# Kernel optimization log

Hardware: AMD Instinct MI355X
Metric: run time of the kernel (lower is better)

Reference implementation:

```python
import jax, jax.numpy as jnp
import numpy as np

B, C, H, W = 16, 192, 64, 64
L = 256           # number of quantization levels (len(sos.unique_values))
EXTREMA = 10.0    # codebook support roughly [-extrema, extrema]


def setup_inputs() -> dict:
    key = jax.random.key(0)
    k1, k2, k3 = jax.random.split(key, 3)
    inputs = jax.random.normal(k1, (B, C, H, W), dtype=jnp.float32) * 3.0
    means = jax.random.normal(k2, (B, C, H, W), dtype=jnp.float32)
    # sorted codebook of unique quantizer output values (sos.unique_values)
    raw = jax.random.uniform(k3, (L,), dtype=jnp.float32,
                             minval=-EXTREMA, maxval=EXTREMA)
    unique_values = jnp.sort(raw)
    return {"inputs": inputs, "means": means, "unique_values": unique_values}


def _nearest_symbols(v, unique_values):
    # Parallel binary search over the sorted codebook; equivalent to the
    # original per-element argmin(|keys - x|) in transform_map.
    L_ = unique_values.shape[0]
    idx = jnp.searchsorted(unique_values, v)          # in [0, L]
    idx = jnp.clip(idx, 1, L_ - 1)
    left = unique_values[idx - 1]
    right = unique_values[idx]
    # on ties, argmin picks the lower index -> use <=
    return jnp.where(jnp.abs(v - left) <= jnp.abs(v - right), idx - 1, idx)


def reference(inputs, means, unique_values):
    # quantize(mode='symbols'): subtract means, snap to nearest codebook
    # value, map value -> integer symbol via the sorted codebook.
    v = inputs - means
    symbols = _nearest_symbols(v, unique_values)      # int32 [B,C,H,W]
    # dequantize: symbol -> float codebook value (map_cdf_sos), add means.
    dequant = unique_values[symbols] + means          # float32 [B,C,H,W]
    return dequant, symbols
```

## Files before the change

### kernel.cpp

```cpp
#include <hip/hip_runtime.h>


#define LVL 256
#define NB  512
#define QPT 4

typedef float f32x4 __attribute__((ext_vector_type(4)));

__device__ __forceinline__ int bucket_of(float v, float lo, float scale) {
    int b = (int)floorf((v - lo) * scale);
    return min(max(b, 0), NB - 1);
}

__global__ __launch_bounds__(256) void agc_build_lut(
    const float* __restrict__ uv, float4* __restrict__ lutA, float4* __restrict__ lutB)
{
    __shared__ float s_uv[LVL];
    __shared__ int   s_b[LVL];
    int t = threadIdx.x;
    s_uv[t] = uv[t];
    __syncthreads();
    const float lo    = s_uv[0];
    const float scale = (float)NB / (s_uv[LVL - 1] - lo);
    s_b[t] = bucket_of(s_uv[t], lo, scale);
    __syncthreads();

    int b = blockIdx.x * 256 + t;
    if (b >= NB) return;

    int A = 0, cnt = 0;
    for (int j = 0; j < LVL; ++j) {
        int bj = s_b[j];
        A   += (bj <  b);
        cnt += (bj == b);
    }

    const float INF = __builtin_inff();
    float4 ea, eb;
    if (cnt == 0) {
        int idx = min(max(A, 1), LVL - 1);
        ea = make_float4(INF, INF, s_uv[idx - 1], s_uv[idx]);
        eb = make_float4(0.f, 0.f, 0.f, __int_as_float(idx - 1));
    } else if (cnt <= 2 && A >= 1 && A + cnt <= LVL - 1) {
        float p0 = s_uv[A];
        float p1 = (cnt >= 2) ? s_uv[A + 1] : INF;
        float c0 = s_uv[A - 1];
        float c1 = s_uv[A];
        float c2 = s_uv[A + 1];
        float c3 = (A + 2 <= LVL - 1) ? s_uv[A + 2] : 0.f;
        ea = make_float4(p0, p1, c0, c1);
        eb = make_float4(c2, c3, 0.f, __int_as_float(A - 1));
    } else {
        ea = make_float4(0.f, 0.f, 0.f, 0.f);
        eb = make_float4(0.f, 0.f, 0.f, __int_as_float(-(A + 1)));
    }
    lutA[b] = ea;
    lutB[b] = eb;
}

__global__ __launch_bounds__(256) void agc_quant_lut(
    const float* __restrict__ inputs,
    const float* __restrict__ means,
    const float* __restrict__ uv,
    const f32x4* __restrict__ lutA,
    const f32x4* __restrict__ lutB,
    float* __restrict__ out_deq,
    float* __restrict__ out_sym,
    int n4, int n, int nfull)
{
    const float lo    = uv[0];
    const float scale = (float)NB / (uv[LVL - 1] - lo);

    int t = threadIdx.x;
    const int i0 = blockIdx.x * (256 * QPT) + t;
    const bool full = (blockIdx.x < nfull);

    f32x4 in[QPT], mn[QPT];
    if (full) {
        #pragma unroll
        for (int k = 0; k < QPT; ++k) {
            int i = i0 + k * 256;
            in[k] = __builtin_nontemporal_load(reinterpret_cast<const f32x4*>(inputs) + i);
            mn[k] = __builtin_nontemporal_load(reinterpret_cast<const f32x4*>(means) + i);
        }
    } else {
        #pragma unroll
        for (int k = 0; k < QPT; ++k) {
            int i = i0 + k * 256;
            if (i < n4) {
                in[k] = __builtin_nontemporal_load(reinterpret_cast<const f32x4*>(inputs) + i);
                mn[k] = __builtin_nontemporal_load(reinterpret_cast<const f32x4*>(means) + i);
            }
        }
    }

    #pragma unroll
    for (int k = 0; k < QPT; ++k) {
        int i = i0 + k * 256;
        if (!full && i >= n4) continue;

        float vs[4] = {in[k].x - mn[k].x, in[k].y - mn[k].y,
                       in[k].z - mn[k].z, in[k].w - mn[k].w};
        float ms[4] = {mn[k].x, mn[k].y, mn[k].z, mn[k].w};
        float dq[4], sy[4];

        int bx[4];
        #pragma unroll
        for (int e = 0; e < 4; ++e) bx[e] = bucket_of(vs[e], lo, scale);

        f32x4 A4[4], B4[4];
        #pragma unroll
        for (int e = 0; e < 4; ++e) {
            A4[e] = lutA[bx[e]];
            B4[e] = lutB[bx[e]];
        }

        #pragma unroll
        for (int e = 0; e < 4; ++e) {
            float v = vs[e];
            int bp = __float_as_int(B4[e].w);

            float left, right;
            int base;
            if (bp >= 0) {
                int sel = (A4[e].x < v) + (A4[e].y < v);
                left  = (sel == 0) ? A4[e].z : ((sel == 1) ? A4[e].w : B4[e].x);
                right = (sel == 0) ? A4[e].w : ((sel == 1) ? B4[e].x : B4[e].y);
                base  = bp + sel;
            } else {
                int s = -bp - 1;
                while (s < LVL && uv[s] < v) ++s;
                int idx = min(max(s, 1), LVL - 1);
                left  = uv[idx - 1];
                right = uv[idx];
                base  = idx - 1;
            }

            bool tl = (fabsf(v - left) <= fabsf(v - right));
            sy[e] = (float)(base + (tl ? 0 : 1));
            dq[e] = (tl ? left : right) + ms[e];
        }

        reinterpret_cast<float4*>(out_deq)[i] = make_float4(dq[0], dq[1], dq[2], dq[3]);
        reinterpret_cast<float4*>(out_sym)[i] = make_float4(sy[0], sy[1], sy[2], sy[3]);
    }

    if (blockIdx.x == 0 && t == 0) {
        for (int j = n4 * 4; j < n; ++j) {
            float m = means[j];
            float v = inputs[j] - m;
            int l = 0, h = LVL;
            for (int s = 0; s < 8; ++s) {
                int mm = (l + h) >> 1;
                bool r = (uv[mm] < v);
                l = r ? (mm + 1) : l;
                h = r ? h : mm;
            }
            int idx = min(max(l, 1), LVL - 1);
            float left = uv[idx - 1], right = uv[idx];
            bool tl = fabsf(v - left) <= fabsf(v - right);
            out_deq[j] = (tl ? left : right) + m;
            out_sym[j] = (float)(tl ? idx - 1 : idx);
        }
    }
}

__global__ __launch_bounds__(256) void agc_quant_fallback(
    const float* __restrict__ inputs,
    const float* __restrict__ means,
    const float* __restrict__ uv,
    float* __restrict__ out_deq,
    float* __restrict__ out_sym,
    int n4, int n)
{
    __shared__ float s_uv[LVL];
    s_uv[threadIdx.x] = uv[threadIdx.x];
    __syncthreads();

    int i = blockIdx.x * blockDim.x + threadIdx.x;
    if (i < n4) {
        float4 in = reinterpret_cast<const float4*>(inputs)[i];
        float4 mn = reinterpret_cast<const float4*>(means)[i];
        float vs[4] = {in.x - mn.x, in.y - mn.y, in.z - mn.z, in.w - mn.w};
        float ms[4] = {mn.x, mn.y, mn.z, mn.w};
        float dq[4], sy[4];
        #pragma unroll
        for (int k = 0; k < 4; ++k) {
            float v = vs[k];
            int lo = 0, hi = LVL;
            #pragma unroll
            for (int s = 0; s < 8; ++s) {
                int mid = (lo + hi) >> 1;
                bool r = (s_uv[mid] < v);
                lo = r ? (mid + 1) : lo;
                hi = r ? hi : mid;
            }
            int idx = min(max(lo, 1), LVL - 1);
            float left = s_uv[idx - 1], right = s_uv[idx];
            bool tl = (fabsf(v - left) <= fabsf(v - right));
            sy[k] = (float)(tl ? idx - 1 : idx);
            dq[k] = (tl ? left : right) + ms[k];
        }
        reinterpret_cast<float4*>(out_deq)[i] = make_float4(dq[0], dq[1], dq[2], dq[3]);
        reinterpret_cast<float4*>(out_sym)[i] = make_float4(sy[0], sy[1], sy[2], sy[3]);
    }
    if (blockIdx.x == 0 && threadIdx.x == 0) {
        for (int j = n4 * 4; j < n; ++j) {
            float m = means[j];
            float v = inputs[j] - m;
            int lo = 0, hi = LVL;
            for (int s = 0; s < 8; ++s) {
                int mid = (lo + hi) >> 1;
                bool r = (s_uv[mid] < v);
                lo = r ? (mid + 1) : lo;
                hi = r ? hi : mid;
            }
            int idx = min(max(lo, 1), LVL - 1);
            float left = s_uv[idx - 1], right = s_uv[idx];
            bool tl = fabsf(v - left) <= fabsf(v - right);
            out_deq[j] = (tl ? left : right) + m;
            out_sym[j] = (float)(tl ? idx - 1 : idx);
        }
    }
}

extern "C" void kernel_launch(void* const* d_in, const int* in_sizes, int n_in,
                              void* d_out, int out_size, void* d_ws, size_t ws_size,
                              hipStream_t stream)
{
    const float* inputs = (const float*)d_in[0];
    const float* means  = (const float*)d_in[1];
    const float* uv     = (const float*)d_in[2];

    int n  = in_sizes[0];
    int n4 = n / 4;

    float* out     = (float*)d_out;
    float* out_deq = out;
    float* out_sym = out + n;

    size_t need = (size_t)NB * 2 * sizeof(float4);
    if (d_ws != nullptr && ws_size >= need) {
        float4* lutA = (float4*)d_ws;
        float4* lutB = lutA + NB;
        agc_build_lut<<<(NB + 255) / 256, 256, 0, stream>>>(uv, lutA, lutB);

        int per_blk = 256 * QPT;
        int nfull   = n4 / per_blk;
        int blocks  = (n4 + per_blk - 1) / per_blk;
        if (blocks < 1) blocks = 1;
        agc_quant_lut<<<blocks, 256, 0, stream>>>(
            inputs, means, uv, (const f32x4*)lutA, (const f32x4*)lutB,
            out_deq, out_sym, n4, n, nfull);
    } else {
        int blocks = (n4 + 255) / 256;
        if (blocks < 1) blocks = 1;
        agc_quant_fallback<<<blocks, 256, 0, stream>>>(
            inputs, means, uv, out_deq, out_sym, n4, n);
    }
}
```

Before: 199.4 us.

## Use single 16-byte bucket LUT with precomputed nearest-pair candidates

Doubles the bucket count and changes the LUT so each bucket stores the two possible nearest codebook values and the base symbol, found by evaluating the exact nearest symbol at the bucket's widened bounds. This halves the per-element table gather (one float4 instead of two) and drops the threshold selection logic. It also replaces nontemporal loads with plain loads and builds the LUT in one block. Risks: a larger table reduces cache locality, and more buckets may fall to the slow linear-scan fallback path if the two-candidate condition fails.

Measured after the change: 202.9 us. Within noise of the previous version (+1.8%).

```diff
diff --git a/kernel.cpp b/kernel.cpp
--- a/kernel.cpp
+++ b/kernel.cpp
@@ -2,7 +2,7 @@
 
 
 #define LVL 256
-#define NB  512
+#define NB  1024
 #define QPT 4
 
 typedef float f32x4 __attribute__((ext_vector_type(4)));
@@ -12,58 +12,74 @@
     return min(max(b, 0), NB - 1);
 }
 
+__device__ __forceinline__ int sym_exact(float x, const float* s_uv) {
+    int l = 0, h = LVL;
+    #pragma unroll
+    for (int s = 0; s < 8; ++s) {
+        int m = (l + h) >> 1;
+        bool r = (s_uv[m] < x);
+        l = r ? (m + 1) : l;
+        h = r ? h : m;
+    }
+    int idx = min(max(l, 1), LVL - 1);
+    float left = s_uv[idx - 1], right = s_uv[idx];
+    return (fabsf(x - left) <= fabsf(x - right)) ? idx - 1 : idx;
+}
+
+__device__ __forceinline__ int lb_count(float x, const float* s_uv) {
+    int l = 0, h = LVL;
+    #pragma unroll
+    for (int s = 0; s < 8; ++s) {
+        int m = (l + h) >> 1;
+        bool r = (s_uv[m] < x);
+        l = r ? (m + 1) : l;
+        h = r ? h : m;
+    }
+    return l;
+}
+
 __global__ __launch_bounds__(256) void agc_build_lut(
-    const float* __restrict__ uv, float4* __restrict__ lutA, float4* __restrict__ lutB)
+    const float* __restrict__ uv, float4* __restrict__ lut)
 {
     __shared__ float s_uv[LVL];
-    __shared__ int   s_b[LVL];
     int t = threadIdx.x;
     s_uv[t] = uv[t];
     __syncthreads();
+
     const float lo    = s_uv[0];
-    const float scale = (float)NB / (s_uv[LVL - 1] - lo);
-    s_b[t] = bucket_of(s_uv[t], lo, scale);
-    __syncthreads();
-
-    int b = blockIdx.x * 256 + t;
-    if (b >= NB) return;
-
-    int A = 0, cnt = 0;
-    for (int j = 0; j < LVL; ++j) {
-        int bj = s_b[j];
-        A   += (bj <  b);
-        cnt += (bj == b);
-    }
-
-    const float INF = __builtin_inff();
-    float4 ea, eb;
-    if (cnt == 0) {
-        int idx = min(max(A, 1), LVL - 1);
-        ea = make_float4(INF, INF, s_uv[idx - 1], s_uv[idx]);
-        eb = make_float4(0.f, 0.f, 0.f, __int_as_float(idx - 1));
-    } else if (cnt <= 2 && A >= 1 && A + cnt <= LVL - 1) {
-        float p0 = s_uv[A];
-        float p1 = (cnt >= 2) ? s_uv[A + 1] : INF;
-        float c0 = s_uv[A - 1];
-        float c1 = s_uv[A];
-        float c2 = s_uv[A + 1];
-        float c3 = (A + 2 <= LVL - 1) ? s_uv[A + 2] : 0.f;
-        ea = make_float4(p0, p1, c0, c1);
-        eb = make_float4(c2, c3, 0.f, __int_as_float(A - 1));
-    } else {
-        ea = make_float4(0.f, 0.f, 0.f, 0.f);
-        eb = make_float4(0.f, 0.f, 0.f, __int_as_float(-(A + 1)));
-    }
-    lutA[b] = ea;
-    lutB[b] = eb;
+    const float rng   = s_uv[LVL - 1] - lo;
+    const float width = rng / (float)NB;
+
+    #pragma unroll
+    for (int q = 0; q < NB / 256; ++q) {
+        int b = q * 256 + t;
+        float g_lo = lo + (float)(b - 1) * width;
+        float g_hi = lo + (float)(b + 2) * width;
+
+        int s1 = (b == 0)      ? 0         : sym_exact(g_lo, s_uv);
+        int s2 = (b == NB - 1) ? (LVL - 1) : sym_exact(g_hi, s_uv);
+
+        float4 e;
+        if (s2 - s1 <= 1) {
+            e.x = s_uv[s1];
+            e.y = s_uv[s2];
+            e.z = __int_as_float(s1);
+            e.w = 0.f;
+        } else {
+            int A = (b == 0) ? 0 : lb_count(g_lo, s_uv);
+            e.x = 0.f; e.y = 0.f;
+            e.z = __int_as_float(-(A + 1));
+            e.w = 0.f;
+        }
+        lut[b] = e;
+    }
 }
 
 __global__ __launch_bounds__(256) void agc_quant_lut(
     const float* __restrict__ inputs,
     const float* __restrict__ means,
     const float* __restrict__ uv,
-    const f32x4* __restrict__ lutA,
-    const f32x4* __restrict__ lutB,
+    const f32x4* __restrict__ lut,
     float* __restrict__ out_deq,
     float* __restrict__ out_sym,
     int n4, int n, int nfull)
@@ -75,21 +91,21 @@
     const int i0 = blockIdx.x * (256 * QPT) + t;
     const bool full = (blockIdx.x < nfull);
 
-    f32x4 in[QPT], mn[QPT];
+    float4 in[QPT], mn[QPT];
     if (full) {
         #pragma unroll
         for (int k = 0; k < QPT; ++k) {
             int i = i0 + k * 256;
-            in[k] = __builtin_nontemporal_load(reinterpret_cast<const f32x4*>(inputs) + i);
-            mn[k] = __builtin_nontemporal_load(reinterpret_cast<const f32x4*>(means) + i);
+            in[k] = reinterpret_cast<const float4*>(inputs)[i];
+            mn[k] = reinterpret_cast<const float4*>(means)[i];
         }
     } else {
         #pragma unroll
         for (int k = 0; k < QPT; ++k) {
             int i = i0 + k * 256;
             if (i < n4) {
-                in[k] = __builtin_nontemporal_load(reinterpret_cast<const f32x4*>(inputs) + i);
-                mn[k] = __builtin_nontemporal_load(reinterpret_cast<const f32x4*>(means) + i);
+                in[k] = reinterpret_cast<const float4*>(inputs)[i];
+                mn[k] = reinterpret_cast<const float4*>(means)[i];
             }
         }
     }
@@ -108,37 +124,33 @@
         #pragma unroll
         for (int e = 0; e < 4; ++e) bx[e] = bucket_of(vs[e], lo, scale);
 
-        f32x4 A4[4], B4[4];
-        #pragma unroll
-        for (int e = 0; e < 4; ++e) {
-            A4[e] = lutA[bx[e]];
-            B4[e] = lutB[bx[e]];
-        }
+        f32x4 E[4];
+        #pragma unroll
+        for (int e = 0; e < 4; ++e) E[e] = lut[bx[e]];
 
         #pragma unroll
         for (int e = 0; e < 4; ++e) {
             float v = vs[e];
-            int bp = __float_as_int(B4[e].w);
-
-            float left, right;
-            int base;
-            if (bp >= 0) {
-                int sel = (A4[e].x < v) + (A4[e].y < v);
-                left  = (sel == 0) ? A4[e].z : ((sel == 1) ? A4[e].w : B4[e].x);
-                right = (sel == 0) ? A4[e].w : ((sel == 1) ? B4[e].x : B4[e].y);
-                base  = bp + sel;
+            int pk = __float_as_int(E[e].z);
+
+            float val; int sym;
+            if (pk >= 0) {
+                bool tl = (fabsf(v - E[e].x) <= fabsf(v - E[e].y));
+                sym = pk + (tl ? 0 : 1);
+                val = tl ? E[e].x : E[e].y;
             } else {
-                int s = -bp - 1;
+                int s = -pk - 1;
                 while (s < LVL && uv[s] < v) ++s;
                 int idx = min(max(s, 1), LVL - 1);
-                left  = uv[idx - 1];
-                right = uv[idx];
-                base  = idx - 1;
-            }
-
-            bool tl = (fabsf(v - left) <= fabsf(v - right));
-            sy[e] = (float)(base + (tl ? 0 : 1));
-            dq[e] = (tl ? left : right) + ms[e];
+                float left  = uv[idx - 1];
+                float right = uv[idx];
+                bool tl = (fabsf(v - left) <= fabsf(v - right));
+                sym = tl ? (idx - 1) : idx;
+                val = tl ? left : right;
+            }
+
+            sy[e] = (float)sym;
+            dq[e] = val + ms[e];
         }
 
         reinterpret_cast<float4*>(out_deq)[i] = make_float4(dq[0], dq[1], dq[2], dq[3]);
@@ -239,18 +251,17 @@
     float* out_deq = out;
     float* out_sym = out + n;
 
-    size_t need = (size_t)NB * 2 * sizeof(float4);
+    size_t need = (size_t)NB * sizeof(float4);
     if (d_ws != nullptr && ws_size >= need) {
-        float4* lutA = (float4*)d_ws;
-        float4* lutB = lutA + NB;
-        agc_build_lut<<<(NB + 255) / 256, 256, 0, stream>>>(uv, lutA, lutB);
+        float4* lut = (float4*)d_ws;
+        agc_build_lut<<<1, 256, 0, stream>>>(uv, lut);
 
         int per_blk = 256 * QPT;
         int nfull   = n4 / per_blk;
         int blocks  = (n4 + per_blk - 1) / per_blk;
         if (blocks < 1) blocks = 1;
         agc_quant_lut<<<blocks, 256, 0, stream>>>(
-            inputs, means, uv, (const f32x4*)lutA, (const f32x4*)lutB,
+            inputs, means, uv, (const f32x4*)lut,
             out_deq, out_sym, n4, n, nfull);
     } else {
         int blocks = (n4 + 255) / 256;
```
